# Performance work log

Hardware: AMD Instinct MI355X
Metric: run time of the kernel (lower is better)

Reference implementation:

```python
import jax, jax.numpy as jnp
import numpy as np

N = 100_000      # nodes
E = 1_600_000    # edges
F_IN = 512       # input node features
H = 128          # hidden (num_hidden)
C = 64           # num_classes


def setup_inputs() -> dict:
    key = jax.random.key(0)
    ks = jax.random.split(key, 16)
    def lin(k, fi, fo):
        return (jax.random.normal(k, (fi, fo), jnp.float32) / np.sqrt(fi)).astype(jnp.float32)
    inp = {
        'x': jax.random.normal(ks[0], (N, F_IN), jnp.float32),
        'edge_index': jax.random.randint(ks[1], (2, E), 0, N, jnp.int32),
        'W0': lin(ks[2], F_IN, H), 'b0': jnp.zeros((H,), jnp.float32),
        'W1': lin(ks[3], H, H),    'b1': jnp.zeros((H,), jnp.float32),
        'W2': lin(ks[4], H, H),    'b2': jnp.zeros((H,), jnp.float32),
        'fc1_w': lin(ks[5], H, H), 'fc1_b': jnp.zeros((H,), jnp.float32),
        'fc2_w': lin(ks[6], H, H), 'fc2_b': jnp.zeros((H,), jnp.float32),
        'fc3_w': lin(ks[7], H, C), 'fc3_b': jnp.zeros((C,), jnp.float32),
    }
    return inp


def _gcn_norm(edge_index):
    # PyG GCNConv: add self-loops, symmetric normalization deg^-1/2 A deg^-1/2
    src = jnp.concatenate([edge_index[0], jnp.arange(N, dtype=edge_index.dtype)])
    dst = jnp.concatenate([edge_index[1], jnp.arange(N, dtype=edge_index.dtype)])
    deg = jax.ops.segment_sum(jnp.ones_like(dst, jnp.float32), dst, num_segments=N)
    dinv = jnp.where(deg > 0, jax.lax.rsqrt(deg), 0.0)
    norm = dinv[src] * dinv[dst]  # [E+N]
    return src, dst, norm


def _gcn_conv(x, W, b, src, dst, norm):
    h = x @ W + b                      # [N, H] transform first (fewer flops when F_in > H)
    msg = h[src] * norm[:, None]       # gather + scale, [E+N, H]
    return jax.ops.segment_sum(msg, dst, num_segments=N)  # scatter-add


def reference(x, edge_index, W0, b0, W1, b1, W2, b2,
              fc1_w, fc1_b, fc2_w, fc2_b, fc3_w, fc3_b):
    src, dst, norm = _gcn_norm(edge_index)
    y = jax.nn.relu(_gcn_conv(x, W0, b0, src, dst, norm))
    y = jax.nn.relu(_gcn_conv(y, W1, b1, src, dst, norm))
    y = jax.nn.relu(_gcn_conv(y, W2, b2, src, dst, norm))
    y = jax.nn.relu(y @ fc1_w + fc1_b)
    y = jax.nn.relu(y @ fc2_w + fc2_b)
    y = y @ fc3_w + fc3_b
    return jax.nn.log_softmax(y, axis=1)
```

## Files before the change

kernel.cpp:

```cpp
#include <hip/hip_runtime.h>
#include <hip/hip_bf16.h>
#include <cstdint>

typedef __hip_bfloat16 bf16;
typedef __hip_bfloat162 bf162;
typedef __bf16 bf16x8 __attribute__((ext_vector_type(8)));
typedef float f32x4 __attribute__((ext_vector_type(4)));

__global__ void detect_kernel(const unsigned short* __restrict__ xr, int* __restrict__ flag) {
  if (threadIdx.x == 0 && blockIdx.x == 0) {
    int pass = 0;
    for (int i = 0; i < 64; ++i) {
      unsigned short h = xr[2 * i];
      int e = (h >> 7) & 0xFF;
      if (e >= 110 && e <= 140) pass++;
    }
    *flag = (pass >= 32) ? 1 : 0;
  }
}

struct CvtDesc {
  const void* src;
  void* dst;
  int n, fi, fo, mode;
};
struct CvtAll { CvtDesc d[12]; };

__global__ void convert_all_kernel(CvtAll all, const int* __restrict__ flag) {
  CvtDesc dd = all.d[blockIdx.y];
  int isbf = *flag;
  for (int i = blockIdx.x * blockDim.x + threadIdx.x; i < dd.n; i += gridDim.x * blockDim.x) {
    float v = isbf ? __bfloat162float(((const bf16*)dd.src)[i]) : ((const float*)dd.src)[i];
    if (dd.mode) {
      int k = i / dd.fo, nn = i - k * dd.fo;
      ((__bf16*)dd.dst)[(size_t)nn * dd.fi + k] = (__bf16)v;
    } else {
      ((float*)dd.dst)[i] = v;
    }
  }
}


__global__ void count_kernel(const int* __restrict__ dst, int* __restrict__ deg, int E) {
  int i = blockIdx.x * blockDim.x + threadIdx.x;
  if (i < E) atomicAdd(&deg[dst[i]], 1);
}

__global__ void dinv_kernel(const int* __restrict__ deg, float* __restrict__ dinv, int n) {
  int i = blockIdx.x * blockDim.x + threadIdx.x;
  if (i < n) dinv[i] = rsqrtf((float)(deg[i] + 1));
}

__global__ void scan_block_kernel(const int* __restrict__ counts, int* __restrict__ excl,
                                  int* __restrict__ bsum, int n) {
  __shared__ int sd[1024];
  int t = threadIdx.x;
  int i = blockIdx.x * 1024 + t;
  int v = (i < n) ? counts[i] : 0;
  sd[t] = v;
  __syncthreads();
  for (int off = 1; off < 1024; off <<= 1) {
    int x = (t >= off) ? sd[t - off] : 0;
    __syncthreads();
    sd[t] += x;
    __syncthreads();
  }
  if (i < n) excl[i] = sd[t] - v;
  if (t == 1023) bsum[blockIdx.x] = sd[1023];
}

__global__ void scan_sums_kernel(int* __restrict__ bsum, int nb, int* __restrict__ row_ptr, int n) {
  __shared__ int sd[1024];
  int t = threadIdx.x;
  int v = (t < nb) ? bsum[t] : 0;
  sd[t] = v;
  __syncthreads();
  for (int off = 1; off < 1024; off <<= 1) {
    int x = (t >= off) ? sd[t - off] : 0;
    __syncthreads();
    sd[t] += x;
    __syncthreads();
  }
  if (t < nb) bsum[t] = sd[t] - v;
  if (t == 1023) row_ptr[n] = sd[1023];
}

__global__ void scan_add_kernel(int* __restrict__ excl, const int* __restrict__ bsum, int n) {
  int i = blockIdx.x * blockDim.x + threadIdx.x;
  if (i < n) excl[i] += bsum[i >> 10];
}

__global__ void fill_kernel(const int* __restrict__ src, const int* __restrict__ dst,
                            const int* __restrict__ row_ptr, int* __restrict__ cursor,
                            int* __restrict__ col, int E) {
  int i = blockIdx.x * blockDim.x + threadIdx.x;
  if (i < E) {
    int d = dst[i];
    int pos = row_ptr[d] + atomicAdd(&cursor[d], 1);
    col[pos] = src[i];
  }
}


template <int K, int ADUAL>
__global__ __launch_bounds__(256) void gemm_mfma_kernel(
    const void* __restrict__ Ain, const __bf16* __restrict__ Bt,
    const float* __restrict__ bias, bf16* __restrict__ C,
    int M, const float* __restrict__ rowscale, int do_relu,
    const int* __restrict__ flag) {
  const int abf = ADUAL ? flag[0] : 1;
  int t = threadIdx.x;
  int wave = t >> 6, lane = t & 63;
  int l15 = lane & 15, quad = lane >> 4;
  int wm = wave >> 1, wn = wave & 1;
  int rowbase = blockIdx.x * 128 + wm * 64;
  int colbase = wn * 64;
  const __bf16* Ab = (const __bf16*)Ain;
  const float* Af = (const float*)Ain;

  f32x4 acc[4][4];
#pragma unroll
  for (int mt = 0; mt < 4; ++mt)
#pragma unroll
    for (int nt = 0; nt < 4; ++nt) acc[mt][nt] = (f32x4){0.f, 0.f, 0.f, 0.f};

  int arow[4];
#pragma unroll
  for (int mt = 0; mt < 4; ++mt) {
    int r = rowbase + mt * 16 + l15;
    arow[mt] = (r < M) ? r : (M - 1);
  }
  int brow[4];
#pragma unroll
  for (int nt = 0; nt < 4; ++nt) brow[nt] = colbase + nt * 16 + l15;

  bf16x8 aA[4], bA[4], aB[4], bB[4];

  auto load_chunk = [&](int kc, bf16x8 (&av)[4], bf16x8 (&bv)[4]) {
    int ko = kc + quad * 8;
    if (abf) {
#pragma unroll
      for (int mt = 0; mt < 4; ++mt)
        av[mt] = *(const bf16x8*)(Ab + (size_t)arow[mt] * K + ko);
    } else {
#pragma unroll
      for (int mt = 0; mt < 4; ++mt) {
        const float* p = Af + (size_t)arow[mt] * K + ko;
#pragma unroll
        for (int j = 0; j < 8; ++j) av[mt][j] = (__bf16)p[j];
      }
    }
#pragma unroll
    for (int nt = 0; nt < 4; ++nt)
      bv[nt] = *(const bf16x8*)(Bt + (size_t)brow[nt] * K + ko);
  };

  auto mfma16 = [&](const bf16x8 (&av)[4], const bf16x8 (&bv)[4]) {
#pragma unroll
    for (int mt = 0; mt < 4; ++mt)
#pragma unroll
      for (int nt = 0; nt < 4; ++nt)
        acc[mt][nt] =
            __builtin_amdgcn_mfma_f32_16x16x32_bf16(av[mt], bv[nt], acc[mt][nt], 0, 0, 0);
  };

  constexpr int NC = K / 32;
  load_chunk(0, aA, bA);
#pragma unroll
  for (int c = 0; c < NC; c += 2) {
    if (c + 1 < NC) load_chunk((c + 1) * 32, aB, bB);
    mfma16(aA, bA);
    if (c + 2 < NC) load_chunk((c + 2) * 32, aA, bA);
    if (c + 1 < NC) mfma16(aB, bB);
  }

#pragma unroll
  for (int mt = 0; mt < 4; ++mt) {
    int r0 = rowbase + mt * 16 + quad * 4;
#pragma unroll
    for (int nt = 0; nt < 4; ++nt) {
      int c = colbase + nt * 16 + l15;
      float bs = bias[c];
#pragma unroll
      for (int i = 0; i < 4; ++i) {
        int r = r0 + i;
        if (r < M) {
          float v = acc[mt][nt][i] + bs;
          if (rowscale) v *= rowscale[r];
          if (do_relu) v = fmaxf(v, 0.f);
          C[(size_t)r * 128 + c] = __float2bfloat16(v);
        }
      }
    }
  }
}


__global__ __launch_bounds__(256) void gather_kernel(
    const bf16* __restrict__ g, const int* __restrict__ row_ptr, const int* __restrict__ col,
    const float* __restrict__ dinv, bf16* __restrict__ y, int n) {
  int wave = threadIdx.x >> 6;
  int lane = threadIdx.x & 63;
  int node = blockIdx.x * 4 + wave;
  if (node >= n) return;
  const bf162* gp = (const bf162*)g;
  bf162 sv = gp[(size_t)node * 64 + lane];
  float ax = __bfloat162float(sv.x), ay = __bfloat162float(sv.y);
  float bx = 0.f, by = 0.f;
  int beg = row_ptr[node], end = row_ptr[node + 1];
  for (int e = beg; e < end; e += 8) {
    int s[8];
    float msk[8];
#pragma unroll
    for (int j = 0; j < 8; ++j) {
      int ee = e + j;
      bool ok = ee < end;
      s[j] = col[ok ? ee : e];
      msk[j] = ok ? 1.f : 0.f;
    }
    bf162 v[8];
#pragma unroll
    for (int j = 0; j < 8; ++j) v[j] = gp[(size_t)s[j] * 64 + lane];
#pragma unroll
    for (int j = 0; j < 8; j += 2) {
      ax = fmaf(msk[j], __bfloat162float(v[j].x), ax);
      ay = fmaf(msk[j], __bfloat162float(v[j].y), ay);
      bx = fmaf(msk[j + 1], __bfloat162float(v[j + 1].x), bx);
      by = fmaf(msk[j + 1], __bfloat162float(v[j + 1].y), by);
    }
  }
  float dv = dinv[node];
  float ox = fmaxf((ax + bx) * dv, 0.f);
  float oy = fmaxf((ay + by) * dv, 0.f);
  bf162 o;
  o.x = __float2bfloat16(ox);
  o.y = __float2bfloat16(oy);
  ((bf162*)y)[(size_t)node * 64 + lane] = o;
}


__global__ __launch_bounds__(256) void fc3_softmax_mfma_kernel(
    const bf16* __restrict__ y, const __bf16* __restrict__ Wt,
    const float* __restrict__ b, void* __restrict__ out, int M,
    const int* __restrict__ flag) {
  const int isbf = flag[0];
  int t = threadIdx.x;
  int wave = t >> 6, lane = t & 63;
  int l15 = lane & 15, quad = lane >> 4;
  int rowbase = blockIdx.x * 256 + wave * 64;

  f32x4 acc[4][4];
#pragma unroll
  for (int mt = 0; mt < 4; ++mt)
#pragma unroll
    for (int nt = 0; nt < 4; ++nt) acc[mt][nt] = (f32x4){0.f, 0.f, 0.f, 0.f};

  int arow[4];
#pragma unroll
  for (int mt = 0; mt < 4; ++mt) {
    int r = rowbase + mt * 16 + l15;
    arow[mt] = (r < M) ? r : (M - 1);
  }

  bf16x8 aA[4], bA[4], aB[4], bB[4];

  auto load_chunk = [&](int kc, bf16x8 (&av)[4], bf16x8 (&bv)[4]) {
    int ko = kc + quad * 8;
#pragma unroll
    for (int mt = 0; mt < 4; ++mt)
      av[mt] = *(const bf16x8*)(y + (size_t)arow[mt] * 128 + ko);
#pragma unroll
    for (int nt = 0; nt < 4; ++nt)
      bv[nt] = *(const bf16x8*)(Wt + (size_t)(nt * 16 + l15) * 128 + ko);
  };

  auto mfma16 = [&](const bf16x8 (&av)[4], const bf16x8 (&bv)[4]) {
#pragma unroll
    for (int mt = 0; mt < 4; ++mt)
#pragma unroll
      for (int nt = 0; nt < 4; ++nt)
        acc[mt][nt] =
            __builtin_amdgcn_mfma_f32_16x16x32_bf16(av[mt], bv[nt], acc[mt][nt], 0, 0, 0);
  };

  load_chunk(0, aA, bA);
  load_chunk(32, aB, bB);
  mfma16(aA, bA);
  load_chunk(64, aA, bA);
  mfma16(aB, bB);
  load_chunk(96, aB, bB);
  mfma16(aA, bA);
  mfma16(aB, bB);

  float bcol[4];
#pragma unroll
  for (int nt = 0; nt < 4; ++nt) bcol[nt] = b[nt * 16 + l15];

#pragma unroll
  for (int mt = 0; mt < 4; ++mt) {
#pragma unroll
    for (int i = 0; i < 4; ++i) {
      int r = rowbase + mt * 16 + quad * 4 + i;
      float v0 = acc[mt][0][i] + bcol[0];
      float v1 = acc[mt][1][i] + bcol[1];
      float v2 = acc[mt][2][i] + bcol[2];
      float v3 = acc[mt][3][i] + bcol[3];
      float m = fmaxf(fmaxf(v0, v1), fmaxf(v2, v3));
#pragma unroll
      for (int off = 8; off > 0; off >>= 1) m = fmaxf(m, __shfl_xor(m, off, 16));
      float s = __expf(v0 - m) + __expf(v1 - m) + __expf(v2 - m) + __expf(v3 - m);
#pragma unroll
      for (int off = 8; off > 0; off >>= 1) s += __shfl_xor(s, off, 16);
      float ls = m + __logf(s);
      if (r < M) {
        if (isbf) {
          bf16* op = (bf16*)out + (size_t)r * 64 + l15;
          op[0] = __float2bfloat16(v0 - ls);
          op[16] = __float2bfloat16(v1 - ls);
          op[32] = __float2bfloat16(v2 - ls);
          op[48] = __float2bfloat16(v3 - ls);
        } else {
          float* op = (float*)out + (size_t)r * 64 + l15;
          op[0] = v0 - ls;
          op[16] = v1 - ls;
          op[32] = v2 - ls;
          op[48] = v3 - ls;
        }
      }
    }
  }
}


extern "C" void kernel_launch(void* const* d_in, const int* in_sizes, int n_in,
                              void* d_out, int out_size, void* d_ws, size_t ws_size,
                              hipStream_t stream) {
  const void* x = d_in[0];
  const int* ei = (const int*)d_in[1];

  const int N = in_sizes[0] / 512;
  const int E = in_sizes[1] / 2;
  const int* srcp = ei;
  const int* dstp = ei + E;

  char* ws = (char*)d_ws;
  size_t off = 0;
  auto alloc = [&](size_t bytes) {
    void* p = ws + off;
    off = (off + bytes + 255) & ~(size_t)255;
    return p;
  };
  int*    flag    = (int*)alloc(4);
  int*    deg     = (int*)alloc((size_t)N * 4);
  int*    cursor  = (int*)alloc((size_t)N * 4);
  int*    row_ptr = (int*)alloc((size_t)(N + 1) * 4);
  int*    col     = (int*)alloc((size_t)E * 4);
  float*  dinv    = (float*)alloc((size_t)N * 4);
  int*    bsum    = (int*)alloc(1024 * 4);
  __bf16* W0t     = (__bf16*)alloc((size_t)512 * 128 * 2);
  __bf16* W1t     = (__bf16*)alloc((size_t)128 * 128 * 2);
  __bf16* W2t     = (__bf16*)alloc((size_t)128 * 128 * 2);
  __bf16* fc1t    = (__bf16*)alloc((size_t)128 * 128 * 2);
  __bf16* fc2t    = (__bf16*)alloc((size_t)128 * 128 * 2);
  __bf16* fc3t    = (__bf16*)alloc((size_t)64 * 128 * 2);
  float*  b0f     = (float*)alloc(128 * 4);
  float*  b1f     = (float*)alloc(128 * 4);
  float*  b2f     = (float*)alloc(128 * 4);
  float*  fc1bf   = (float*)alloc(128 * 4);
  float*  fc2bf   = (float*)alloc(128 * 4);
  float*  fc3bf   = (float*)alloc(64 * 4);
  bf16*   gbuf    = (bf16*)alloc((size_t)N * 128 * 2);
  bf16*   ybuf    = (bf16*)alloc((size_t)N * 128 * 2);

  const int tb = 256;

  detect_kernel<<<1, 64, 0, stream>>>((const unsigned short*)x, flag);

  CvtAll ca;
  ca.d[0]  = {d_in[2],  W0t,   512 * 128, 512, 128, 1};
  ca.d[1]  = {d_in[4],  W1t,   128 * 128, 128, 128, 1};
  ca.d[2]  = {d_in[6],  W2t,   128 * 128, 128, 128, 1};
  ca.d[3]  = {d_in[8],  fc1t,  128 * 128, 128, 128, 1};
  ca.d[4]  = {d_in[10], fc2t,  128 * 128, 128, 128, 1};
  ca.d[5]  = {d_in[3],  b0f,   128, 0, 0, 0};
  ca.d[6]  = {d_in[5],  b1f,   128, 0, 0, 0};
  ca.d[7]  = {d_in[7],  b2f,   128, 0, 0, 0};
  ca.d[8]  = {d_in[9],  fc1bf, 128, 0, 0, 0};
  ca.d[9]  = {d_in[11], fc2bf, 128, 0, 0, 0};
  ca.d[10] = {d_in[12], fc3t,  128 * 64, 128, 64, 1};
  ca.d[11] = {d_in[13], fc3bf, 64, 0, 0, 0};
  convert_all_kernel<<<dim3(64, 12), 256, 0, stream>>>(ca, flag);

  hipMemsetAsync(deg, 0, (size_t)N * 4, stream);
  hipMemsetAsync(cursor, 0, (size_t)N * 4, stream);

  count_kernel<<<(E + tb - 1) / tb, tb, 0, stream>>>(dstp, deg, E);
  dinv_kernel<<<(N + tb - 1) / tb, tb, 0, stream>>>(deg, dinv, N);
  int nb = (N + 1023) / 1024;
  scan_block_kernel<<<nb, 1024, 0, stream>>>(deg, row_ptr, bsum, N);
  scan_sums_kernel<<<1, 1024, 0, stream>>>(bsum, nb, row_ptr, N);
  scan_add_kernel<<<(N + tb - 1) / tb, tb, 0, stream>>>(row_ptr, bsum, N);
  fill_kernel<<<(E + tb - 1) / tb, tb, 0, stream>>>(srcp, dstp, row_ptr, cursor, col, E);

  int gemm_blocks = (N + 127) / 128;
  int gat_blocks = (N + 3) / 4;
  int fc3_blocks = (N + 255) / 256;

  gemm_mfma_kernel<512, 1><<<gemm_blocks, 256, 0, stream>>>(x, W0t, b0f, gbuf, N, dinv, 0, flag);
  gather_kernel<<<gat_blocks, 256, 0, stream>>>(gbuf, row_ptr, col, dinv, ybuf, N);
  gemm_mfma_kernel<128, 0><<<gemm_blocks, 256, 0, stream>>>(ybuf, W1t, b1f, gbuf, N, dinv, 0, flag);
  gather_kernel<<<gat_blocks, 256, 0, stream>>>(gbuf, row_ptr, col, dinv, ybuf, N);
  gemm_mfma_kernel<128, 0><<<gemm_blocks, 256, 0, stream>>>(ybuf, W2t, b2f, gbuf, N, dinv, 0, flag);
  gather_kernel<<<gat_blocks, 256, 0, stream>>>(gbuf, row_ptr, col, dinv, ybuf, N);
  gemm_mfma_kernel<128, 0><<<gemm_blocks, 256, 0, stream>>>(ybuf, fc1t, fc1bf, gbuf, N, nullptr, 1, flag);
  gemm_mfma_kernel<128, 0><<<gemm_blocks, 256, 0, stream>>>(gbuf, fc2t, fc2bf, ybuf, N, nullptr, 1, flag);
  fc3_softmax_mfma_kernel<<<fc3_blocks, 256, 0, stream>>>(ybuf, fc3t, fc3bf, d_out, N, flag);
}
```

Baseline: 870.2 us.

## Stage GEMM tiles through double-buffered swizzled LDS with global_load_lds

The MFMA GEMM kernel now stages 128x64 tiles of A and B into double-buffered shared memory using direct global-to-LDS loads, with an XOR swizzle to avoid bank conflicts. Previously each wave loaded its fragments straight from global memory, so A and B rows were fetched redundantly by the waves sharing them. This adds 64KB of LDS per block and a barrier per k-tile, which may lower occupancy. The fp32 input path converts in registers and writes to LDS with ordinary stores.

```diff
diff --git a/kernel.cpp b/kernel.cpp
--- a/kernel.cpp
+++ b/kernel.cpp
@@ -101,6 +101,12 @@
   }
 }
 
+__device__ __forceinline__ void gload_lds16(const void* g, void* l) {
+  __builtin_amdgcn_global_load_lds(
+      (const __attribute__((address_space(1))) void*)g,
+      (__attribute__((address_space(3))) void*)l, 16, 0, 0);
+}
+
 
 template <int K, int ADUAL>
 __global__ __launch_bounds__(256) void gemm_mfma_kernel(
@@ -108,78 +114,99 @@
     const float* __restrict__ bias, bf16* __restrict__ C,
     int M, const float* __restrict__ rowscale, int do_relu,
     const int* __restrict__ flag) {
+  constexpr int BK = 64;
+  constexpr int NT = K / BK;
+  __shared__ __align__(16) __bf16 As[2][128 * BK];
+  __shared__ __align__(16) __bf16 Bs[2][128 * BK];
+
   const int abf = ADUAL ? flag[0] : 1;
   int t = threadIdx.x;
   int wave = t >> 6, lane = t & 63;
   int l15 = lane & 15, quad = lane >> 4;
   int wm = wave >> 1, wn = wave & 1;
-  int rowbase = blockIdx.x * 128 + wm * 64;
-  int colbase = wn * 64;
+  int rowbase = blockIdx.x * 128;
   const __bf16* Ab = (const __bf16*)Ain;
   const float* Af = (const float*)Ain;
 
+  int srow = t >> 3;
+  int sslot = t & 7;
+  int xslot = sslot ^ (srow & 7);
+
+  int sArow[4];
+#pragma unroll
+  for (int i = 0; i < 4; ++i) {
+    int r = rowbase + i * 32 + srow;
+    sArow[i] = (r < M) ? r : (M - 1);
+  }
+
   f32x4 acc[4][4];
 #pragma unroll
   for (int mt = 0; mt < 4; ++mt)
 #pragma unroll
     for (int nt = 0; nt < 4; ++nt) acc[mt][nt] = (f32x4){0.f, 0.f, 0.f, 0.f};
 
-  int arow[4];
+  auto stage = [&](int kt, int buf) {
+    int kbase = kt * BK + xslot * 8;
+    if (abf) {
+#pragma unroll
+      for (int i = 0; i < 4; ++i)
+        gload_lds16(Ab + (size_t)sArow[i] * K + kbase, &As[buf][t * 8 + i * 2048]);
+    } else {
+#pragma unroll
+      for (int i = 0; i < 4; ++i) {
+        const float* p = Af + (size_t)sArow[i] * K + kbase;
+        bf16x8 v;
+#pragma unroll
+        for (int j = 0; j < 8; ++j) v[j] = (__bf16)p[j];
+        *(bf16x8*)&As[buf][t * 8 + i * 2048] = v;
+      }
+    }
+#pragma unroll
+    for (int i = 0; i < 4; ++i)
+      gload_lds16(Bt + (size_t)(i * 32 + srow) * K + kbase, &Bs[buf][t * 8 + i * 2048]);
+  };
+
+  auto compute = [&](int buf) {
+#pragma unroll
+    for (int c = 0; c < 2; ++c) {
+      bf16x8 av[4], bv[4];
+#pragma unroll
+      for (int mt = 0; mt < 4; ++mt) {
+        int row = wm * 64 + mt * 16 + l15;
+        int slot = (c * 4 + quad) ^ (row & 7);
+        av[mt] = *(const bf16x8*)&As[buf][row * BK + slot * 8];
+      }
+#pragma unroll
+      for (int nt = 0; nt < 4; ++nt) {
+        int row = wn * 64 + nt * 16 + l15;
+        int slot = (c * 4 + quad) ^ (row & 7);
+        bv[nt] = *(const bf16x8*)&Bs[buf][row * BK + slot * 8];
+      }
+#pragma unroll
+      for (int mt = 0; mt < 4; ++mt)
+#pragma unroll
+        for (int nt = 0; nt < 4; ++nt)
+          acc[mt][nt] =
+              __builtin_amdgcn_mfma_f32_16x16x32_bf16(av[mt], bv[nt], acc[mt][nt], 0, 0, 0);
+    }
+  };
+
+  stage(0, 0);
+  __syncthreads();
+#pragma unroll
+  for (int kt = 0; kt < NT; ++kt) {
+    int cur = kt & 1;
+    if (kt + 1 < NT) stage(kt + 1, cur ^ 1);
+    compute(cur);
+    __syncthreads();
+  }
+
 #pragma unroll
   for (int mt = 0; mt < 4; ++mt) {
-    int r = rowbase + mt * 16 + l15;
-    arow[mt] = (r < M) ? r : (M - 1);
-  }
-  int brow[4];
-#pragma unroll
-  for (int nt = 0; nt < 4; ++nt) brow[nt] = colbase + nt * 16 + l15;
-
-  bf16x8 aA[4], bA[4], aB[4], bB[4];
-
-  auto load_chunk = [&](int kc, bf16x8 (&av)[4], bf16x8 (&bv)[4]) {
-    int ko = kc + quad * 8;
-    if (abf) {
-#pragma unroll
-      for (int mt = 0; mt < 4; ++mt)
-        av[mt] = *(const bf16x8*)(Ab + (size_t)arow[mt] * K + ko);
-    } else {
-#pragma unroll
-      for (int mt = 0; mt < 4; ++mt) {
-        const float* p = Af + (size_t)arow[mt] * K + ko;
-#pragma unroll
-        for (int j = 0; j < 8; ++j) av[mt][j] = (__bf16)p[j];
-      }
-    }
-#pragma unroll
-    for (int nt = 0; nt < 4; ++nt)
-      bv[nt] = *(const bf16x8*)(Bt + (size_t)brow[nt] * K + ko);
-  };
-
-  auto mfma16 = [&](const bf16x8 (&av)[4], const bf16x8 (&bv)[4]) {
-#pragma unroll
-    for (int mt = 0; mt < 4; ++mt)
-#pragma unroll
-      for (int nt = 0; nt < 4; ++nt)
-        acc[mt][nt] =
-            __builtin_amdgcn_mfma_f32_16x16x32_bf16(av[mt], bv[nt], acc[mt][nt], 0, 0, 0);
-  };
-
-  constexpr int NC = K / 32;
-  load_chunk(0, aA, bA);
-#pragma unroll
-  for (int c = 0; c < NC; c += 2) {
-    if (c + 1 < NC) load_chunk((c + 1) * 32, aB, bB);
-    mfma16(aA, bA);
-    if (c + 2 < NC) load_chunk((c + 2) * 32, aA, bA);
-    if (c + 1 < NC) mfma16(aB, bB);
-  }
-
-#pragma unroll
-  for (int mt = 0; mt < 4; ++mt) {
-    int r0 = rowbase + mt * 16 + quad * 4;
+    int r0 = rowbase + wm * 64 + mt * 16 + quad * 4;
 #pragma unroll
     for (int nt = 0; nt < 4; ++nt) {
-      int c = colbase + nt * 16 + l15;
+      int c = wn * 64 + nt * 16 + l15;
       float bs = bias[c];
 #pragma unroll
       for (int i = 0; i < 4; ++i) {
```

New measurement: 828.2 us. 4.8% less time.
